# Performance work log

Measured on AMD Instinct MI355X. Metric: run time of the kernel, lower is better.

## Reference

```python
import jax, jax.numpy as jnp
import numpy as np

D_MODEL = 1024
N_HEADS = 16
D_HEAD = D_MODEL // N_HEADS


def setup_inputs() -> dict:
    key = jax.random.key(0)
    ks = jax.random.split(key, 5)
    B, T = 2, 2048
    x = jax.random.normal(ks[0], (B, T, D_MODEL), dtype=jnp.float32)
    s = 1.0 / np.sqrt(D_MODEL)
    W_qkv = jax.random.normal(ks[1], (D_MODEL, 3 * D_MODEL), dtype=jnp.float32) * s
    b_qkv = jnp.zeros((3 * D_MODEL,), dtype=jnp.float32)
    W_proj = jax.random.normal(ks[2], (D_MODEL, D_MODEL), dtype=jnp.float32) * s
    b_proj = jnp.zeros((D_MODEL,), dtype=jnp.float32)
    return {"x": x, "W_qkv": W_qkv, "b_qkv": b_qkv, "W_proj": W_proj, "b_proj": b_proj}


def reference(x, W_qkv, b_qkv, W_proj, b_proj):
    B, T, C = x.shape
    qkv = x @ W_qkv + b_qkv                      # [B,T,3C]
    q, k, v = jnp.split(qkv, 3, axis=-1)
    # [B,T,C] -> [B,H,T,Dh]
    def to_heads(t):
        return t.reshape(B, T, N_HEADS, D_HEAD).transpose(0, 2, 1, 3)
    q, k, v = to_heads(q), to_heads(k), to_heads(v)
    scale = 1.0 / np.sqrt(D_HEAD).astype(np.float32)
    scores = jnp.einsum('bhqd,bhkd->bhqk', q, k) * scale  # [B,H,T,T]
    causal = jnp.tril(jnp.ones((T, T), dtype=bool))
    scores = jnp.where(causal, scores, -jnp.inf)
    attn = jax.nn.softmax(scores, axis=-1)
    out = jnp.einsum('bhqk,bhkd->bhqd', attn, v)          # [B,H,T,Dh]
    out = out.transpose(0, 2, 1, 3).reshape(B, T, C)
    return out @ W_proj + b_proj
```

## Files before the change

kernel.cpp:

```cpp
#include <hip/hip_runtime.h>
#include <hip/hip_bf16.h>
#include <cstdint>


using u16 = unsigned short;
using u32 = unsigned int;

typedef __bf16 bf16x8 __attribute__((ext_vector_type(8)));
typedef float f32x4 __attribute__((ext_vector_type(4)));

#define AS1 __attribute__((address_space(1)))
#define AS3 __attribute__((address_space(3)))

__device__ __forceinline__ u16 f2bf(float f) {
  u32 u = __float_as_uint(f);
  u += 0x7fffu + ((u >> 16) & 1u);
  return (u16)(u >> 16);
}
__device__ __forceinline__ u32 cvtpk(float a, float b) {
  u32 r;
  asm("v_cvt_pk_bf16_f32 %0, %1, %2" : "=v"(r) : "v"(a), "v"(b));
  return r;
}

__global__ __launch_bounds__(256) void prep(const float* __restrict__ x,
                                            u16* __restrict__ xb,
                                            const float* __restrict__ W0,
                                            u16* __restrict__ T0,
                                            const float* __restrict__ W1,
                                            u16* __restrict__ T1) {
  const int bx = blockIdx.x;
  const int tid = threadIdx.x;
  if (bx < 4096) {
    const int i = bx * 256 + tid;
    float4 v = ((const float4*)x)[i];
    ushort4 o;
    o.x = f2bf(v.x); o.y = f2bf(v.y); o.z = f2bf(v.z); o.w = f2bf(v.w);
    ((ushort4*)xb)[i] = o;
    return;
  }
  __shared__ float t[32][33];
  const int idx = bx - 4096;
  const int bxx = idx & 127, by = idx >> 7;
  const float* W; u16* Wt; int N, n0;
  if (bxx < 96) { W = W0; Wt = T0; N = 3072; n0 = bxx * 32; }
  else          { W = W1; Wt = T1; N = 1024; n0 = (bxx - 96) * 32; }
  const int k0 = by * 32;
  const int tx = tid & 31, ty = tid >> 5;
#pragma unroll
  for (int i = 0; i < 4; ++i)
    t[ty + i * 8][tx] = W[(size_t)(k0 + ty + i * 8) * N + n0 + tx];
  __syncthreads();
#pragma unroll
  for (int i = 0; i < 4; ++i)
    Wt[(size_t)(n0 + ty + i * 8) * 1024 + k0 + tx] = f2bf(t[tx][ty + i * 8]);
}

#define MFMA16 __builtin_amdgcn_mfma_f32_16x16x32_bf16

__global__ __launch_bounds__(512, 2) void gemm_qkv(const u16* __restrict__ A,
                                                   const u16* __restrict__ Bt,
                                                   const float* __restrict__ bias,
                                                   u16* __restrict__ qb,
                                                   u16* __restrict__ KF,
                                                   u16* __restrict__ VF,
                                                   float sc_val) {
  constexpr int NT = 16;
  constexpr int BUFO = 7 * 4096;
  __shared__ __align__(16) u16 sm[2 * BUFO];

  const int tid  = threadIdx.x;
  const int lane = tid & 63;
  const int w    = tid >> 6;
  const int quad = lane >> 4;
  const int l15  = lane & 15;

  const int bid = blockIdx.x;
  const int xcd = bid & 7, c = bid >> 3;
  const int mt = (xcd >> 1) * 4 + (c & 3);
  const int nt = (xcd & 1) * 8 + (c >> 2);
  const int bm = mt * 256, bn = nt * 192;

  const int wr = (w >> 2) * 128;
  const int wc = (w & 3) * 48;

  const int srow = tid >> 3;
  const int scol = (((tid & 7) ^ ((tid >> 3) & 7)) << 3);

#define STAGEA(ch, ktile, bufo)                                                 \
  __builtin_amdgcn_global_load_lds(                                             \
      (AS1 const void*)(A + (size_t)(bm + (ch) * 64 + srow) * 1024 +            \
                        ((ktile) << 6) + scol),                                 \
      (AS3 void*)(sm + (bufo) + (ch) * 4096 + tid * 8), 16, 0, 0)
#define STAGEB(ch, ktile, bufo)                                                 \
  __builtin_amdgcn_global_load_lds(                                             \
      (AS1 const void*)(Bt + (size_t)(bn + (ch) * 64 + srow) * 1024 +           \
                        ((ktile) << 6) + scol),                                 \
      (AS3 void*)(sm + (bufo) + (4 + (ch)) * 4096 + tid * 8), 16, 0, 0)

  const int ca = (w >> 2) * 2;
  int abase_lo[4], abase_hi[4], bbase[3];
#pragma unroll
  for (int mi = 0; mi < 4; ++mi) {
    abase_lo[mi] = (ca + 0) * 4096 + (mi * 16 + l15) * 64;
    abase_hi[mi] = (ca + 1) * 4096 + (mi * 16 + l15) * 64;
  }
#pragma unroll
  for (int ni = 0; ni < 3; ++ni) {
    const int rb = wc + ni * 16 + l15;
    bbase[ni] = (4 + (rb >> 6)) * 4096 + (rb & 63) * 64;
  }
  const int sw0 = ((quad ^ (l15 & 7)) << 3);
  const int sw1 = sw0 ^ 32;

  STAGEA(0, 0, 0); STAGEA(1, 0, 0); STAGEA(2, 0, 0); STAGEA(3, 0, 0);
  STAGEB(0, 0, 0); STAGEB(1, 0, 0); STAGEB(2, 0, 0);
  STAGEB(0, 1, BUFO); STAGEB(1, 1, BUFO);
  STAGEB(2, 1, BUFO); STAGEA(0, 1, BUFO); STAGEA(1, 1, BUFO);
  asm volatile("s_waitcnt vmcnt(5)" ::: "memory");
  __builtin_amdgcn_s_barrier();

  f32x4 acc[8][3] = {};
  bf16x8 alo[4][2], ahi[4][2], b[3][2];

#pragma unroll 2
  for (int j = 0; j < NT; ++j) {
    const int bo  = (j & 1) * BUFO;
    const int nbo = bo ^ BUFO;
    const u16* smb = sm + bo;

#pragma unroll
    for (int mi = 0; mi < 4; ++mi) {
      alo[mi][0] = *(const bf16x8*)(smb + abase_lo[mi] + sw0);
      alo[mi][1] = *(const bf16x8*)(smb + abase_lo[mi] + sw1);
    }
#pragma unroll
    for (int ni = 0; ni < 2; ++ni) {
      b[ni][0] = *(const bf16x8*)(smb + bbase[ni] + sw0);
      b[ni][1] = *(const bf16x8*)(smb + bbase[ni] + sw1);
    }
#pragma unroll
    for (int mi = 0; mi < 4; ++mi) {
      ahi[mi][0] = *(const bf16x8*)(smb + abase_hi[mi] + sw0);
      ahi[mi][1] = *(const bf16x8*)(smb + abase_hi[mi] + sw1);
    }
    b[2][0] = *(const bf16x8*)(smb + bbase[2] + sw0);
    b[2][1] = *(const bf16x8*)(smb + bbase[2] + sw1);
    if (j + 1 < NT) { STAGEA(2, j + 1, nbo); STAGEA(3, j + 1, nbo); }

    asm volatile("s_waitcnt lgkmcnt(10)" ::: "memory");
    __builtin_amdgcn_sched_barrier(0);
    __builtin_amdgcn_s_setprio(1);
#pragma unroll
    for (int mi = 0; mi < 4; ++mi)
#pragma unroll
      for (int ni = 0; ni < 2; ++ni) {
        acc[mi][ni] = MFMA16(alo[mi][0], b[ni][0], acc[mi][ni], 0, 0, 0);
        acc[mi][ni] = MFMA16(alo[mi][1], b[ni][1], acc[mi][ni], 0, 0, 0);
      }
    __builtin_amdgcn_s_setprio(0);
    asm volatile("s_waitcnt lgkmcnt(0)" ::: "memory");
    __builtin_amdgcn_sched_barrier(0);
    __builtin_amdgcn_s_barrier();
    if (j + 2 < NT) {
      STAGEB(0, j + 2, bo); STAGEB(1, j + 2, bo); STAGEB(2, j + 2, bo);
      STAGEA(0, j + 2, bo); STAGEA(1, j + 2, bo);
    }
    __builtin_amdgcn_s_setprio(1);
#pragma unroll
    for (int mi = 0; mi < 4; ++mi) {
      acc[mi][2] = MFMA16(alo[mi][0], b[2][0], acc[mi][2], 0, 0, 0);
      acc[mi][2] = MFMA16(alo[mi][1], b[2][1], acc[mi][2], 0, 0, 0);
      acc[4 + mi][0] = MFMA16(ahi[mi][0], b[0][0], acc[4 + mi][0], 0, 0, 0);
      acc[4 + mi][0] = MFMA16(ahi[mi][1], b[0][1], acc[4 + mi][0], 0, 0, 0);
    }
#pragma unroll
    for (int mi = 0; mi < 4; ++mi)
#pragma unroll
      for (int ni = 1; ni < 3; ++ni) {
        acc[4 + mi][ni] = MFMA16(ahi[mi][0], b[ni][0], acc[4 + mi][ni], 0, 0, 0);
        acc[4 + mi][ni] = MFMA16(ahi[mi][1], b[ni][1], acc[4 + mi][ni], 0, 0, 0);
      }
    __builtin_amdgcn_s_setprio(0);
    if (j + 2 < NT)
      asm volatile("s_waitcnt vmcnt(5)" ::: "memory");
    else
      asm volatile("s_waitcnt vmcnt(0)" ::: "memory");
    __builtin_amdgcn_s_barrier();
  }
#undef STAGEA
#undef STAGEB

  const int crow0 = bm + wr + (quad << 2);
  const int ccol0 = bn + wc + l15;
#pragma unroll
  for (int ni = 0; ni < 3; ++ni) {
    const int n = ccol0 + ni * 16;
    const float bv = bias[n];
    if (n < 1024) {
#pragma unroll
      for (int mi = 0; mi < 8; ++mi) {
        const int m0 = crow0 + mi * 16;
#pragma unroll
        for (int r = 0; r < 4; ++r)
          qb[(size_t)(m0 + r) * 1024 + n] = f2bf((acc[mi][ni][r] + bv) * sc_val);
      }
    } else if (n < 2048) {
      const int hk = (n - 1024) >> 6;
      const int d  = (n - 1024) & 63;
      const int hh = d >> 5, qd = (d >> 3) & 3, jj = d & 7;
#pragma unroll
      for (int mi = 0; mi < 8; ++mi) {
#pragma unroll
        for (int r = 0; r < 4; ++r) {
          const int t  = crow0 + mi * 16 + r;
          const int bb = t >> 11, tt = t & 2047;
          const int kt = tt >> 6, mm = (tt >> 4) & 3, l = tt & 15;
          KF[((size_t)((bb * 16 + hk) * 32 + kt) * 8 + mm * 2 + hh) * 512 +
             (qd * 16 + l) * 8 + jj] = f2bf(acc[mi][ni][r] + bv);
        }
      }
    } else {
      const int hv = (n - 2048) >> 6;
      const int d  = (n - 2048) & 63;
      const int di = d >> 4, l = d & 15;
#pragma unroll
      for (int mi = 0; mi < 8; ++mi) {
#pragma unroll
        for (int r = 0; r < 4; ++r) {
          const int t  = crow0 + mi * 16 + r;
          const int bb = t >> 11, tt = t & 2047;
          const int kt = tt >> 6, to = tt & 63;
          const int mq = to >> 4, qd2 = (to >> 2) & 3, rr = to & 3;
          const int hh = mq >> 1, jj = (mq & 1) * 4 + rr;
          VF[((size_t)((bb * 16 + hv) * 32 + kt) * 8 + hh * 4 + di) * 512 +
             (qd2 * 16 + l) * 8 + jj] = f2bf(acc[mi][ni][r] + bv);
        }
      }
    }
  }
}

__global__ __launch_bounds__(256, 2) void gemm_proj(const u16* __restrict__ A,
                                                    const u16* __restrict__ Bt,
                                                    const float* __restrict__ bias,
                                                    float* __restrict__ C) {
  constexpr int NT = 16;
  constexpr int BUFO = 4 * 4096;
  __shared__ __align__(16) u16 sm[2 * BUFO];

  const int tid  = threadIdx.x;
  const int lane = tid & 63;
  const int w    = tid >> 6;
  const int quad = lane >> 4;
  const int l15  = lane & 15;

  const int bid = blockIdx.x;
  const int xcd = bid & 7, c = bid >> 3;
  const int mt = xcd * 4 + (c & 3);
  const int nt = c >> 2;
  const int bm = mt * 128, bn = nt * 128;

  const int wr = (w >> 1) * 64;
  const int wcC = (w & 1) * 64;

  const int srow = tid >> 3;
  const int scol = (((tid & 7) ^ ((tid >> 3) & 7)) << 3);

#define PSTAGEA(ch, ktile, bufo)                                                \
  do {                                                                          \
    const u16* _s = A + (size_t)(bm + (ch) * 64 + srow) * 1024 +                \
                    ((ktile) << 6) + scol;                                      \
    u16* _d = sm + (bufo) + (ch) * 4096 + tid * 8;                              \
    __builtin_amdgcn_global_load_lds((AS1 const void*)_s, (AS3 void*)_d,        \
                                     16, 0, 0);                                 \
    __builtin_amdgcn_global_load_lds((AS1 const void*)(_s + (32 << 10)),        \
                                     (AS3 void*)(_d + 2048), 16, 0, 0);         \
  } while (0)
#define PSTAGEB(ch, ktile, bufo)                                                \
  do {                                                                          \
    const u16* _s = Bt + (size_t)(bn + (ch) * 64 + srow) * 1024 +               \
                    ((ktile) << 6) + scol;                                      \
    u16* _d = sm + (bufo) + (2 + (ch)) * 4096 + tid * 8;                        \
    __builtin_amdgcn_global_load_lds((AS1 const void*)_s, (AS3 void*)_d,        \
                                     16, 0, 0);                                 \
    __builtin_amdgcn_global_load_lds((AS1 const void*)(_s + (32 << 10)),        \
                                     (AS3 void*)(_d + 2048), 16, 0, 0);         \
  } while (0)

  int abase[4], bbase[4];
#pragma unroll
  for (int mi = 0; mi < 4; ++mi)
    abase[mi] = (w >> 1) * 4096 + (mi * 16 + l15) * 64;
#pragma unroll
  for (int ni = 0; ni < 4; ++ni)
    bbase[ni] = (2 + (w & 1)) * 4096 + (ni * 16 + l15) * 64;
  const int sw0 = ((quad ^ (l15 & 7)) << 3);
  const int sw1 = sw0 ^ 32;

  PSTAGEA(0, 0, 0); PSTAGEA(1, 0, 0);
  PSTAGEB(0, 0, 0); PSTAGEB(1, 0, 0);
  PSTAGEA(0, 1, BUFO); PSTAGEA(1, 1, BUFO);
  asm volatile("s_waitcnt vmcnt(4)" ::: "memory");
  __builtin_amdgcn_s_barrier();

  f32x4 acc[4][4] = {};
  bf16x8 a[4][2], b[4][2];

#pragma unroll 2
  for (int j = 0; j < NT; ++j) {
    const int bo  = (j & 1) * BUFO;
    const int nbo = bo ^ BUFO;
    const u16* smb = sm + bo;

#pragma unroll
    for (int mi = 0; mi < 4; ++mi) {
      a[mi][0] = *(const bf16x8*)(smb + abase[mi] + sw0);
      a[mi][1] = *(const bf16x8*)(smb + abase[mi] + sw1);
    }
#pragma unroll
    for (int ni = 0; ni < 2; ++ni) {
      b[ni][0] = *(const bf16x8*)(smb + bbase[ni] + sw0);
      b[ni][1] = *(const bf16x8*)(smb + bbase[ni] + sw1);
    }
#pragma unroll
    for (int ni = 2; ni < 4; ++ni) {
      b[ni][0] = *(const bf16x8*)(smb + bbase[ni] + sw0);
      b[ni][1] = *(const bf16x8*)(smb + bbase[ni] + sw1);
    }
    if (j + 1 < NT) { PSTAGEB(0, j + 1, nbo); PSTAGEB(1, j + 1, nbo); }

    asm volatile("s_waitcnt lgkmcnt(4)" ::: "memory");
    __builtin_amdgcn_sched_barrier(0);
    __builtin_amdgcn_s_setprio(1);
#pragma unroll
    for (int mi = 0; mi < 4; ++mi)
#pragma unroll
      for (int ni = 0; ni < 2; ++ni) {
        acc[mi][ni] = MFMA16(a[mi][0], b[ni][0], acc[mi][ni], 0, 0, 0);
        acc[mi][ni] = MFMA16(a[mi][1], b[ni][1], acc[mi][ni], 0, 0, 0);
      }
    __builtin_amdgcn_s_setprio(0);
    asm volatile("s_waitcnt lgkmcnt(0)" ::: "memory");
    __builtin_amdgcn_sched_barrier(0);
    __builtin_amdgcn_s_barrier();
    if (j + 2 < NT) { PSTAGEA(0, j + 2, bo); PSTAGEA(1, j + 2, bo); }
    __builtin_amdgcn_s_setprio(1);
#pragma unroll
    for (int mi = 0; mi < 4; ++mi)
#pragma unroll
      for (int ni = 2; ni < 4; ++ni) {
        acc[mi][ni] = MFMA16(a[mi][0], b[ni][0], acc[mi][ni], 0, 0, 0);
        acc[mi][ni] = MFMA16(a[mi][1], b[ni][1], acc[mi][ni], 0, 0, 0);
      }
    __builtin_amdgcn_s_setprio(0);
    if (j + 2 < NT)
      asm volatile("s_waitcnt vmcnt(4)" ::: "memory");
    else
      asm volatile("s_waitcnt vmcnt(0)" ::: "memory");
    __builtin_amdgcn_s_barrier();
  }
#undef PSTAGEA
#undef PSTAGEB

  const int crow0 = bm + wr + (quad << 2);
  const int ccol0 = bn + wcC + l15;
#pragma unroll
  for (int ni = 0; ni < 4; ++ni) {
    const int n = ccol0 + ni * 16;
    const float bv = bias[n];
#pragma unroll
    for (int mi = 0; mi < 4; ++mi) {
      const int m0 = crow0 + mi * 16;
#pragma unroll
      for (int r = 0; r < 4; ++r)
        C[(size_t)(m0 + r) * 1024 + n] = acc[mi][ni][r] + bv;
    }
  }
}

__global__ __launch_bounds__(128, 2) void attn_bal(const u16* __restrict__ qb,
                                                   const u16* __restrict__ KF,
                                                   const u16* __restrict__ VF,
                                                   u16* __restrict__ out) {
  const int bid = blockIdx.x;
  const int c   = bid >> 3;
  const int u   = c & 31;
  const int bh  = (bid & 7) | ((c >> 5) << 3);
  const int b = bh >> 4, h = bh & 15;
  const int tid = threadIdx.x;
  const int lane = tid & 63;
  const int par  = tid >> 6;
  const int quad = lane >> 4;
  const int l15  = lane & 15;

  __shared__ float CB[64][41];

  const u16* qbase = qb + (size_t)b * 2048 * 1024 + h * 64;
  const size_t fb = (size_t)bh * 32 * 4096 + lane * 8;
  const u16* kfb = KF + fb;
  const u16* vfb = VF + fb;

  union { u32 u4[4]; bf16x8 v; } onesu;
  onesu.u4[0] = onesu.u4[1] = onesu.u4[2] = onesu.u4[3] = 0x3f803f80u;
  const bf16x8 onesf = onesu.v;

  u16* const outb = out + (size_t)b * 2048 * 1024 + h * 64 + l15;

  auto run_group = [&](int g32) {
    const int q0 = g32 * 32;
    const int ktmax = g32 >> 1;

    bf16x8 qf[2][2];
#pragma unroll
    for (int g = 0; g < 2; ++g)
#pragma unroll
      for (int hh = 0; hh < 2; ++hh)
        qf[g][hh] = *(const bf16x8*)(qbase + (size_t)(q0 + g * 16 + l15) * 1024 +
                                     hh * 32 + quad * 8);

    f32x4 accO[2][4] = {};
    f32x4 accL[2] = {};

    bf16x8 kA[4][2], kB[4][2], vA[2][4], vB[2][4];
    {
      const u16* kp = kfb + (size_t)par * 4096;
      const u16* vp = vfb + (size_t)par * 4096;
#pragma unroll
      for (int m = 0; m < 4; ++m)
#pragma unroll
        for (int hh = 0; hh < 2; ++hh)
          kA[m][hh] = *(const bf16x8*)(kp + (m * 2 + hh) * 512);
#pragma unroll
      for (int hh = 0; hh < 2; ++hh)
#pragma unroll
        for (int di = 0; di < 4; ++di)
          vA[hh][di] = *(const bf16x8*)(vp + (hh * 4 + di) * 512);
    }

    auto tile = [&](int kt, bf16x8 (&KC)[4][2], bf16x8 (&KN)[4][2],
                    bf16x8 (&VC)[2][4], bf16x8 (&VN)[2][4]) {
      const int ktn = (kt + 2 <= ktmax) ? kt + 2 : ktmax;
      const u16* kpn = kfb + (size_t)ktn * 4096;
      const u16* vpn = vfb + (size_t)ktn * 4096;
#pragma unroll
      for (int m = 0; m < 4; ++m)
#pragma unroll
        for (int hh = 0; hh < 2; ++hh)
          KN[m][hh] = *(const bf16x8*)(kpn + (m * 2 + hh) * 512);
#pragma unroll
      for (int hh = 0; hh < 2; ++hh)
#pragma unroll
        for (int di = 0; di < 4; ++di)
          VN[hh][di] = *(const bf16x8*)(vpn + (hh * 4 + di) * 512);

      const bool diag = (kt == ktmax);
      bf16x8 ap[2][2];
#pragma unroll
      for (int g = 0; g < 2; ++g) {
        f32x4 sT[4] = {};
#pragma unroll
        for (int m = 0; m < 4; ++m) {
          sT[m] = MFMA16(KC[m][0], qf[g][0], sT[m], 0, 0, 0);
          sT[m] = MFMA16(KC[m][1], qf[g][1], sT[m], 0, 0, 0);
        }
        float pv[4][4];
        if (diag) {
          const int qgl = q0 + g * 16 + l15;
#pragma unroll
          for (int m = 0; m < 4; ++m)
#pragma unroll
            for (int r = 0; r < 4; ++r) {
              const bool msk = (kt * 64 + m * 16 + quad * 4 + r) > qgl;
              pv[m][r] = msk ? 0.f : __builtin_amdgcn_exp2f(sT[m][r]);
            }
        } else {
#pragma unroll
          for (int m = 0; m < 4; ++m)
#pragma unroll
            for (int r = 0; r < 4; ++r)
              pv[m][r] = __builtin_amdgcn_exp2f(sT[m][r]);
        }
        union { u32 u4[4]; bf16x8 v; } t0, t1;
        t0.u4[0] = cvtpk(pv[0][0], pv[0][1]);
        t0.u4[1] = cvtpk(pv[0][2], pv[0][3]);
        t0.u4[2] = cvtpk(pv[1][0], pv[1][1]);
        t0.u4[3] = cvtpk(pv[1][2], pv[1][3]);
        t1.u4[0] = cvtpk(pv[2][0], pv[2][1]);
        t1.u4[1] = cvtpk(pv[2][2], pv[2][3]);
        t1.u4[2] = cvtpk(pv[3][0], pv[3][1]);
        t1.u4[3] = cvtpk(pv[3][2], pv[3][3]);
        ap[g][0] = t0.v;
        ap[g][1] = t1.v;
      }

#pragma unroll
      for (int hh = 0; hh < 2; ++hh)
#pragma unroll
        for (int di = 0; di < 4; ++di) {
          bf16x8 bv = VC[hh][di];
#pragma unroll
          for (int g = 0; g < 2; ++g)
            accO[g][di] = MFMA16(ap[g][hh], bv, accO[g][di], 0, 0, 0);
        }
#pragma unroll
      for (int g = 0; g < 2; ++g) {
        accL[g] = MFMA16(ap[g][0], onesf, accL[g], 0, 0, 0);
        accL[g] = MFMA16(ap[g][1], onesf, accL[g], 0, 0, 0);
      }
    };

    for (int kt = par; kt <= ktmax; ) {
      tile(kt, kA, kB, vA, vB); kt += 2;
      if (kt > ktmax) break;
      tile(kt, kB, kA, vB, vA); kt += 2;
    }

    if (par) {
      float* cb = CB[lane];
#pragma unroll
      for (int g = 0; g < 2; ++g) {
#pragma unroll
        for (int di = 0; di < 4; ++di)
#pragma unroll
          for (int r = 0; r < 4; ++r)
            cb[g * 16 + di * 4 + r] = accO[g][di][r];
#pragma unroll
        for (int r = 0; r < 4; ++r)
          cb[32 + g * 4 + r] = accL[g][r];
      }
    }
    __syncthreads();
    if (!par) {
      const float* cb = CB[lane];
#pragma unroll
      for (int g = 0; g < 2; ++g) {
#pragma unroll
        for (int di = 0; di < 4; ++di)
#pragma unroll
          for (int r = 0; r < 4; ++r)
            accO[g][di][r] += cb[g * 16 + di * 4 + r];
#pragma unroll
        for (int r = 0; r < 4; ++r)
          accL[g][r] += cb[32 + g * 4 + r];
      }
#pragma unroll
      for (int g = 0; g < 2; ++g)
#pragma unroll
        for (int r = 0; r < 4; ++r) {
          const float inv = 1.f / accL[g][r];
          const int q = q0 + g * 16 + quad * 4 + r;
          u16* op = outb + (size_t)q * 1024;
#pragma unroll
          for (int di = 0; di < 4; ++di)
            op[di * 16] = f2bf(accO[g][di][r] * inv);
        }
    }
    __syncthreads();
  };

  run_group(63 - u);
  run_group(u);
}

extern "C" void kernel_launch(void* const* d_in, const int* in_sizes, int n_in,
                              void* d_out, int out_size, void* d_ws, size_t ws_size,
                              hipStream_t stream) {
  const float* x     = (const float*)d_in[0];
  const float* Wqkv  = (const float*)d_in[1];
  const float* bqkv  = (const float*)d_in[2];
  const float* Wproj = (const float*)d_in[3];
  const float* bproj = (const float*)d_in[4];
  float* out = (float*)d_out;

  char* ws = (char*)d_ws;
  u16* xb     = (u16*)(ws);
  u16* wqkvT  = (u16*)(ws + 8388608);
  u16* wprojT = (u16*)(ws + 14680064);
  u16* qb     = (u16*)(ws + 16777216);
  u16* KF     = (u16*)(ws + 25165824);
  u16* VF     = (u16*)(ws + 33554432);
  u16* att    = (u16*)(ws + 41943040);

  constexpr float cs = 0.18033688011f;

  prep<<<8192, 256, 0, stream>>>(x, xb, Wqkv, wqkvT, Wproj, wprojT);

  gemm_qkv<<<dim3(256), 512, 0, stream>>>(xb, wqkvT, bqkv, qb, KF, VF, cs);

  attn_bal<<<dim3(1024), 128, 0, stream>>>(qb, KF, VF, att);

  gemm_proj<<<dim3(256), 256, 0, stream>>>(att, wprojT, bproj, out);
}
```

Baseline: 154.8 us.

## Shrink GEMM tiles to double block counts for QKV and projection GEMMs

Result: faster. 149.6 us (-3.4%).

```diff
diff --git a/kernel.cpp b/kernel.cpp
--- a/kernel.cpp
+++ b/kernel.cpp
@@ -58,7 +58,7 @@
 
 #define MFMA16 __builtin_amdgcn_mfma_f32_16x16x32_bf16
 
-__global__ __launch_bounds__(512, 2) void gemm_qkv(const u16* __restrict__ A,
+__global__ __launch_bounds__(256, 2) void gemm_qkv(const u16* __restrict__ A,
                                                    const u16* __restrict__ Bt,
                                                    const float* __restrict__ bias,
                                                    u16* __restrict__ qb,
@@ -66,7 +66,7 @@
                                                    u16* __restrict__ VF,
                                                    float sc_val) {
   constexpr int NT = 16;
-  constexpr int BUFO = 7 * 4096;
+  constexpr int BUFO = 5 * 4096;
   __shared__ __align__(16) u16 sm[2 * BUFO];
 
   const int tid  = threadIdx.x;
@@ -77,47 +77,54 @@
 
   const int bid = blockIdx.x;
   const int xcd = bid & 7, c = bid >> 3;
-  const int mt = (xcd >> 1) * 4 + (c & 3);
-  const int nt = (xcd & 1) * 8 + (c >> 2);
-  const int bm = mt * 256, bn = nt * 192;
-
-  const int wr = (w >> 2) * 128;
-  const int wc = (w & 3) * 48;
+  const int mt = xcd * 4 + (c & 3);
+  const int nt = c >> 2;
+  const int bm = mt * 128, bn = nt * 192;
+
+  const int wc = w * 48;
 
   const int srow = tid >> 3;
   const int scol = (((tid & 7) ^ ((tid >> 3) & 7)) << 3);
 
 #define STAGEA(ch, ktile, bufo)                                                 \
-  __builtin_amdgcn_global_load_lds(                                             \
-      (AS1 const void*)(A + (size_t)(bm + (ch) * 64 + srow) * 1024 +            \
-                        ((ktile) << 6) + scol),                                 \
-      (AS3 void*)(sm + (bufo) + (ch) * 4096 + tid * 8), 16, 0, 0)
+  do {                                                                          \
+    const u16* _s = A + (size_t)(bm + (ch) * 64 + srow) * 1024 +                \
+                    ((ktile) << 6) + scol;                                      \
+    u16* _d = sm + (bufo) + (ch) * 4096 + tid * 8;                              \
+    __builtin_amdgcn_global_load_lds((AS1 const void*)_s, (AS3 void*)_d,        \
+                                     16, 0, 0);                                 \
+    __builtin_amdgcn_global_load_lds((AS1 const void*)(_s + (32 << 10)),        \
+                                     (AS3 void*)(_d + 2048), 16, 0, 0);         \
+  } while (0)
 #define STAGEB(ch, ktile, bufo)                                                 \
-  __builtin_amdgcn_global_load_lds(                                             \
-      (AS1 const void*)(Bt + (size_t)(bn + (ch) * 64 + srow) * 1024 +           \
-                        ((ktile) << 6) + scol),                                 \
-      (AS3 void*)(sm + (bufo) + (4 + (ch)) * 4096 + tid * 8), 16, 0, 0)
-
-  const int ca = (w >> 2) * 2;
+  do {                                                                          \
+    const u16* _s = Bt + (size_t)(bn + (ch) * 64 + srow) * 1024 +               \
+                    ((ktile) << 6) + scol;                                      \
+    u16* _d = sm + (bufo) + (2 + (ch)) * 4096 + tid * 8;                        \
+    __builtin_amdgcn_global_load_lds((AS1 const void*)_s, (AS3 void*)_d,        \
+                                     16, 0, 0);                                 \
+    __builtin_amdgcn_global_load_lds((AS1 const void*)(_s + (32 << 10)),        \
+                                     (AS3 void*)(_d + 2048), 16, 0, 0);         \
+  } while (0)
+
   int abase_lo[4], abase_hi[4], bbase[3];
 #pragma unroll
   for (int mi = 0; mi < 4; ++mi) {
-    abase_lo[mi] = (ca + 0) * 4096 + (mi * 16 + l15) * 64;
-    abase_hi[mi] = (ca + 1) * 4096 + (mi * 16 + l15) * 64;
+    abase_lo[mi] = 0 * 4096 + (mi * 16 + l15) * 64;
+    abase_hi[mi] = 1 * 4096 + (mi * 16 + l15) * 64;
   }
 #pragma unroll
   for (int ni = 0; ni < 3; ++ni) {
     const int rb = wc + ni * 16 + l15;
-    bbase[ni] = (4 + (rb >> 6)) * 4096 + (rb & 63) * 64;
+    bbase[ni] = (2 + (rb >> 6)) * 4096 + (rb & 63) * 64;
   }
   const int sw0 = ((quad ^ (l15 & 7)) << 3);
   const int sw1 = sw0 ^ 32;
 
-  STAGEA(0, 0, 0); STAGEA(1, 0, 0); STAGEA(2, 0, 0); STAGEA(3, 0, 0);
+  STAGEA(0, 0, 0); STAGEA(1, 0, 0);
   STAGEB(0, 0, 0); STAGEB(1, 0, 0); STAGEB(2, 0, 0);
-  STAGEB(0, 1, BUFO); STAGEB(1, 1, BUFO);
-  STAGEB(2, 1, BUFO); STAGEA(0, 1, BUFO); STAGEA(1, 1, BUFO);
-  asm volatile("s_waitcnt vmcnt(5)" ::: "memory");
+  STAGEA(0, 1, BUFO); STAGEA(1, 1, BUFO);
+  asm volatile("s_waitcnt vmcnt(4)" ::: "memory");
   __builtin_amdgcn_s_barrier();
 
   f32x4 acc[8][3] = {};
@@ -146,7 +153,7 @@
     }
     b[2][0] = *(const bf16x8*)(smb + bbase[2] + sw0);
     b[2][1] = *(const bf16x8*)(smb + bbase[2] + sw1);
-    if (j + 1 < NT) { STAGEA(2, j + 1, nbo); STAGEA(3, j + 1, nbo); }
+    if (j + 1 < NT) { STAGEB(0, j + 1, nbo); STAGEB(1, j + 1, nbo); STAGEB(2, j + 1, nbo); }
 
     asm volatile("s_waitcnt lgkmcnt(10)" ::: "memory");
     __builtin_amdgcn_sched_barrier(0);
@@ -162,10 +169,7 @@
     asm volatile("s_waitcnt lgkmcnt(0)" ::: "memory");
     __builtin_amdgcn_sched_barrier(0);
     __builtin_amdgcn_s_barrier();
-    if (j + 2 < NT) {
-      STAGEB(0, j + 2, bo); STAGEB(1, j + 2, bo); STAGEB(2, j + 2, bo);
-      STAGEA(0, j + 2, bo); STAGEA(1, j + 2, bo);
-    }
+    if (j + 2 < NT) { STAGEA(0, j + 2, bo); STAGEA(1, j + 2, bo); }
     __builtin_amdgcn_s_setprio(1);
 #pragma unroll
     for (int mi = 0; mi < 4; ++mi) {
@@ -183,7 +187,7 @@
       }
     __builtin_amdgcn_s_setprio(0);
     if (j + 2 < NT)
-      asm volatile("s_waitcnt vmcnt(5)" ::: "memory");
+      asm volatile("s_waitcnt vmcnt(4)" ::: "memory");
     else
       asm volatile("s_waitcnt vmcnt(0)" ::: "memory");
     __builtin_amdgcn_s_barrier();
@@ -191,7 +195,7 @@
 #undef STAGEA
 #undef STAGEB
 
-  const int crow0 = bm + wr + (quad << 2);
+  const int crow0 = bm + (quad << 2);
   const int ccol0 = bn + wc + l15;
 #pragma unroll
   for (int ni = 0; ni < 3; ++ni) {
@@ -246,7 +250,7 @@
                                                     const float* __restrict__ bias,
                                                     float* __restrict__ C) {
   constexpr int NT = 16;
-  constexpr int BUFO = 4 * 4096;
+  constexpr int BUFO = 3 * 4096;
   __shared__ __align__(16) u16 sm[2 * BUFO];
 
   const int tid  = threadIdx.x;
@@ -259,10 +263,10 @@
   const int xcd = bid & 7, c = bid >> 3;
   const int mt = xcd * 4 + (c & 3);
   const int nt = c >> 2;
-  const int bm = mt * 128, bn = nt * 128;
+  const int bm = mt * 128, bn = nt * 64;
 
   const int wr = (w >> 1) * 64;
-  const int wcC = (w & 1) * 64;
+  const int wcC = (w & 1) * 32;
 
   const int srow = tid >> 3;
   const int scol = (((tid & 7) ^ ((tid >> 3) & 7)) << 3);
@@ -277,35 +281,33 @@
     __builtin_amdgcn_global_load_lds((AS1 const void*)(_s + (32 << 10)),        \
                                      (AS3 void*)(_d + 2048), 16, 0, 0);         \
   } while (0)
-#define PSTAGEB(ch, ktile, bufo)                                                \
+#define PSTAGEB(ktile, bufo)                                                    \
   do {                                                                          \
-    const u16* _s = Bt + (size_t)(bn + (ch) * 64 + srow) * 1024 +               \
-                    ((ktile) << 6) + scol;                                      \
-    u16* _d = sm + (bufo) + (2 + (ch)) * 4096 + tid * 8;                        \
+    const u16* _s = Bt + (size_t)(bn + srow) * 1024 + ((ktile) << 6) + scol;    \
+    u16* _d = sm + (bufo) + 2 * 4096 + tid * 8;                                 \
     __builtin_amdgcn_global_load_lds((AS1 const void*)_s, (AS3 void*)_d,        \
                                      16, 0, 0);                                 \
     __builtin_amdgcn_global_load_lds((AS1 const void*)(_s + (32 << 10)),        \
                                      (AS3 void*)(_d + 2048), 16, 0, 0);         \
   } while (0)
 
-  int abase[4], bbase[4];
+  int abase[4], bbase[2];
 #pragma unroll
   for (int mi = 0; mi < 4; ++mi)
     abase[mi] = (w >> 1) * 4096 + (mi * 16 + l15) * 64;
 #pragma unroll
-  for (int ni = 0; ni < 4; ++ni)
-    bbase[ni] = (2 + (w & 1)) * 4096 + (ni * 16 + l15) * 64;
+  for (int ni = 0; ni < 2; ++ni)
+    bbase[ni] = 2 * 4096 + (wcC + ni * 16 + l15) * 64;
   const int sw0 = ((quad ^ (l15 & 7)) << 3);
   const int sw1 = sw0 ^ 32;
 
-  PSTAGEA(0, 0, 0); PSTAGEA(1, 0, 0);
-  PSTAGEB(0, 0, 0); PSTAGEB(1, 0, 0);
+  PSTAGEA(0, 0, 0); PSTAGEA(1, 0, 0); PSTAGEB(0, 0);
   PSTAGEA(0, 1, BUFO); PSTAGEA(1, 1, BUFO);
   asm volatile("s_waitcnt vmcnt(4)" ::: "memory");
   __builtin_amdgcn_s_barrier();
 
-  f32x4 acc[4][4] = {};
-  bf16x8 a[4][2], b[4][2];
+  f32x4 acc[4][2] = {};
+  bf16x8 a[4][2], b[2][2];
 
 #pragma unroll 2
   for (int j = 0; j < NT; ++j) {
@@ -323,23 +325,16 @@
       b[ni][0] = *(const bf16x8*)(smb + bbase[ni] + sw0);
       b[ni][1] = *(const bf16x8*)(smb + bbase[ni] + sw1);
     }
-#pragma unroll
-    for (int ni = 2; ni < 4; ++ni) {
-      b[ni][0] = *(const bf16x8*)(smb + bbase[ni] + sw0);
-      b[ni][1] = *(const bf16x8*)(smb + bbase[ni] + sw1);
-    }
-    if (j + 1 < NT) { PSTAGEB(0, j + 1, nbo); PSTAGEB(1, j + 1, nbo); }
-
-    asm volatile("s_waitcnt lgkmcnt(4)" ::: "memory");
+    if (j + 1 < NT) PSTAGEB(j + 1, nbo);
+
+    asm volatile("s_waitcnt lgkmcnt(2)" ::: "memory");
     __builtin_amdgcn_sched_barrier(0);
     __builtin_amdgcn_s_setprio(1);
 #pragma unroll
-    for (int mi = 0; mi < 4; ++mi)
-#pragma unroll
-      for (int ni = 0; ni < 2; ++ni) {
-        acc[mi][ni] = MFMA16(a[mi][0], b[ni][0], acc[mi][ni], 0, 0, 0);
-        acc[mi][ni] = MFMA16(a[mi][1], b[ni][1], acc[mi][ni], 0, 0, 0);
-      }
+    for (int mi = 0; mi < 4; ++mi) {
+      acc[mi][0] = MFMA16(a[mi][0], b[0][0], acc[mi][0], 0, 0, 0);
+      acc[mi][0] = MFMA16(a[mi][1], b[0][1], acc[mi][0], 0, 0, 0);
+    }
     __builtin_amdgcn_s_setprio(0);
     asm volatile("s_waitcnt lgkmcnt(0)" ::: "memory");
     __builtin_amdgcn_sched_barrier(0);
@@ -347,12 +342,10 @@
     if (j + 2 < NT) { PSTAGEA(0, j + 2, bo); PSTAGEA(1, j + 2, bo); }
     __builtin_amdgcn_s_setprio(1);
 #pragma unroll
-    for (int mi = 0; mi < 4; ++mi)
-#pragma unroll
-      for (int ni = 2; ni < 4; ++ni) {
-        acc[mi][ni] = MFMA16(a[mi][0], b[ni][0], acc[mi][ni], 0, 0, 0);
-        acc[mi][ni] = MFMA16(a[mi][1], b[ni][1], acc[mi][ni], 0, 0, 0);
-      }
+    for (int mi = 0; mi < 4; ++mi) {
+      acc[mi][1] = MFMA16(a[mi][0], b[1][0], acc[mi][1], 0, 0, 0);
+      acc[mi][1] = MFMA16(a[mi][1], b[1][1], acc[mi][1], 0, 0, 0);
+    }
     __builtin_amdgcn_s_setprio(0);
     if (j + 2 < NT)
       asm volatile("s_waitcnt vmcnt(4)" ::: "memory");
@@ -366,7 +359,7 @@
   const int crow0 = bm + wr + (quad << 2);
   const int ccol0 = bn + wcC + l15;
 #pragma unroll
-  for (int ni = 0; ni < 4; ++ni) {
+  for (int ni = 0; ni < 2; ++ni) {
     const int n = ccol0 + ni * 16;
     const float bv = bias[n];
 #pragma unroll
@@ -586,9 +579,9 @@
 
   prep<<<8192, 256, 0, stream>>>(x, xb, Wqkv, wqkvT, Wproj, wprojT);
 
-  gemm_qkv<<<dim3(256), 512, 0, stream>>>(xb, wqkvT, bqkv, qb, KF, VF, cs);
+  gemm_qkv<<<dim3(512), 256, 0, stream>>>(xb, wqkvT, bqkv, qb, KF, VF, cs);
 
   attn_bal<<<dim3(1024), 128, 0, stream>>>(qb, KF, VF, att);
 
-  gemm_proj<<<dim3(256), 256, 0, stream>>>(att, wprojT, bproj, out);
-}
+  gemm_proj<<<dim3(512), 256, 0, stream>>>(att, wprojT, bproj, out);
+}
```
